# Performance work log

Measured on AMD Instinct MI355X. Metric: run time of the kernel, lower is better.

Reference implementation:

```python
import jax, jax.numpy as jnp
import numpy as np

D_MODEL = 256
NHEAD = 8
HEAD_DIM = D_MODEL // NHEAD
LN_EPS = 1e-5
NEG_INF = -1e30  # finite large-negative; avoids NaN rows while matching masked softmax


def setup_inputs() -> dict:
    key = jax.random.key(0)
    ks = jax.random.split(key, 9)
    B, Q, HW, D = 8, 100, 16384, D_MODEL
    s = 0.02
    return {
        "query": jax.random.normal(ks[0], (B, Q, D), jnp.float32),
        "key_value": jax.random.normal(ks[1], (B, HW, D), jnp.float32),
        "attn_mask": jax.random.randint(ks[2], (B * NHEAD, Q, HW), 0, 2) == 1,  # True = attend
        "in_proj_weight": jax.random.normal(ks[3], (3 * D, D), jnp.float32) * s,
        "in_proj_bias": jax.random.normal(ks[4], (3 * D,), jnp.float32) * s,
        "out_proj_weight": jax.random.normal(ks[5], (D, D), jnp.float32) * s,
        "out_proj_bias": jax.random.normal(ks[6], (D,), jnp.float32) * s,
        "ln_weight": jnp.ones((D,), jnp.float32),
        "ln_bias": jnp.zeros((D,), jnp.float32),
    }


def _mha_masked(query, key_value, attn_mask, in_proj_weight, in_proj_bias,
                out_proj_weight, out_proj_bias):
    B, Q, D = query.shape
    HW = key_value.shape[1]
    Wq, Wk, Wv = jnp.split(in_proj_weight, 3, axis=0)
    bq, bk, bv = jnp.split(in_proj_bias, 3, axis=0)
    q = (query @ Wq.T + bq).reshape(B, Q, NHEAD, HEAD_DIM)
    k = (key_value @ Wk.T + bk).reshape(B, HW, NHEAD, HEAD_DIM)
    v = (key_value @ Wv.T + bv).reshape(B, HW, NHEAD, HEAD_DIM)
    scale = 1.0 / np.sqrt(HEAD_DIM).astype(np.float32)
    scores = jnp.einsum("bqhd,bkhd->bhqk", q, k) * scale  # (B, H, Q, HW)
    attend = attn_mask.reshape(B, NHEAD, Q, HW)  # True = attend
    scores = jnp.where(attend, scores, NEG_INF)
    probs = jax.nn.softmax(scores, axis=-1)
    ctx = jnp.einsum("bhqk,bkhd->bqhd", probs, v).reshape(B, Q, D)
    return ctx @ out_proj_weight.T + out_proj_bias


def reference(query, key_value, attn_mask, in_proj_weight, in_proj_bias,
              out_proj_weight, out_proj_bias, ln_weight, ln_bias):
    attn_out = _mha_masked(query, key_value, attn_mask, in_proj_weight,
                           in_proj_bias, out_proj_weight, out_proj_bias)
    x = query + attn_out  # dropout p=0.0 is identity
    mu = jnp.mean(x, axis=-1, keepdims=True)
    var = jnp.mean(jnp.square(x - mu), axis=-1, keepdims=True)
    return (x - mu) * jax.lax.rsqrt(var + LN_EPS) * ln_weight + ln_bias
```

## Files before the change

### kernel.cpp

```cpp
#include <hip/hip_runtime.h>
#include <stdint.h>

#define BB   8
#define NH   8
#define QQ   100
#define HWK  16384
#define DM   256
#define HD   32
#define QP   112
#define MT   7
#define NPART 64
#define SCALE2 0.2550602534365564f

typedef short bf16x8 __attribute__((ext_vector_type(8)));
typedef float f32x4  __attribute__((ext_vector_type(4)));
typedef unsigned short u16;
typedef unsigned int   u32;
typedef unsigned long long u64;

__device__ __forceinline__ u16 f2bf(float f) {
  u32 u = __builtin_bit_cast(u32, f);
  u += 0x7fffu + ((u >> 16) & 1u);
  return (u16)(u >> 16);
}
__device__ __forceinline__ u16 f2bf_ru(float f) {
  return (u16)((__builtin_bit_cast(u32, f) + 0x8000u) >> 16);
}
__device__ __forceinline__ u32 pack2rn(float lo, float hi) {
  u32 a = __builtin_bit_cast(u32, lo) + 0x8000u;
  u32 b = __builtin_bit_cast(u32, hi) + 0x8000u;
  return __builtin_amdgcn_perm(b, a, 0x07060302u);
}
__device__ __forceinline__ float bf_lo(u32 u) {
  return __builtin_bit_cast(float, u << 16);
}
__device__ __forceinline__ float bf_hi(u32 u) {
  return __builtin_bit_cast(float, u & 0xffff0000u);
}
__device__ __forceinline__ float fast_exp2(float x) {
#if __has_builtin(__builtin_amdgcn_exp2f)
  return __builtin_amdgcn_exp2f(x);
#else
  return exp2f(x);
#endif
}

__global__ __launch_bounds__(256) void qw_kernel(
    const float* __restrict__ query, const float* __restrict__ W,
    const float* __restrict__ bias, u16* __restrict__ q_bf,
    u16* __restrict__ wbf) {
  __shared__ float xrow[DM];
  const int bid = blockIdx.x;
  const int tid = threadIdx.x;
  if (bid >= BB * QQ) {
    const int i = ((bid - BB * QQ) * 256 + tid) * 4;
    const float4 w = *(const float4*)(W + 256 * DM + i);
    u32* dst = (u32*)(wbf + i);
    dst[0] = pack2rn(w.x, w.y);
    dst[1] = pack2rn(w.z, w.w);
    return;
  }
  const int bq = bid;
  const int b = bq / QQ, qi = bq % QQ;
  if (tid < 64)
    ((float4*)xrow)[tid] = ((const float4*)(query + (size_t)bq * DM))[tid];
  __syncthreads();
  const int j = tid;
  float acc = bias[j];
  const float4* wr = (const float4*)(W + (size_t)j * DM);
  #pragma unroll 8
  for (int c = 0; c < 64; ++c) {
    float4 w = wr[c];
    float4 x = ((const float4*)xrow)[c];
    acc += w.x * x.x + w.y * x.y + w.z * x.z + w.w * x.w;
  }
  acc *= SCALE2;
  const int h = j >> 5, d = j & 31;
  q_bf[(((size_t)(b * NH + h)) * QQ + qi) * HD + d] = f2bf(acc);
}

__global__ __launch_bounds__(256) void kvcp_kernel(
    const float* __restrict__ kv, const u16* __restrict__ wbf,
    const float* __restrict__ bias, const int* __restrict__ mask,
    u16* __restrict__ k_bf, u16* __restrict__ v_t, u32* __restrict__ mbg) {
  __shared__ u16 Tl[4][5120];
  const int bid = blockIdx.x;
  const int tid = threadIdx.x, lane = tid & 63, wid = tid >> 6;

  if (bid % 3 == 2) {
    const int cpid = bid / 3;
    const int bh = cpid >> 4, chunk = cpid & 15;
    const int* mp_base = mask + (size_t)bh * QQ * HWK + chunk * 1024;
    u32* dst_base = mbg + (size_t)cpid * QP * 32;
    for (int rr = 0; rr < 25; ++rr) {
      const int row = wid * 25 + rr;
      const int* mp = mp_base + (size_t)row * HWK;
      int4 v[4];
      #pragma unroll
      for (int q = 0; q < 4; ++q) v[q] = ((const int4*)(mp + q * 256))[lane];
      #pragma unroll
      for (int q = 0; q < 4; ++q) {
        const u64 b0 = __ballot(v[q].x != 0);
        const u64 b1 = __ballot(v[q].y != 0);
        const u64 b2 = __ballot(v[q].z != 0);
        const u64 b3 = __ballot(v[q].w != 0);
        if (lane < 8) {
          const int j = lane >> 1;
          const u64 bj = (j == 0) ? b0 : (j == 1) ? b1 : (j == 2) ? b2 : b3;
          dst_base[row * 32 + q * 8 + (lane & 1) * 4 + j] =
              (lane & 1) ? (u32)(bj >> 32) : (u32)bj;
        }
      }
    }
    return;
  }

  const int rb = (bid / 3) * 2 + (bid % 3);
  const size_t m0 = (size_t)rb * 64;
  const int lane15 = lane & 15, quad = lane >> 4;
  const int jw = wid * 128;

  f32x4 acc[4][8];
  #pragma unroll
  for (int mi = 0; mi < 4; ++mi)
    #pragma unroll
    for (int ni = 0; ni < 8; ++ni) acc[mi][ni] = (f32x4){0.f, 0.f, 0.f, 0.f};

  for (int ks = 0; ks < 8; ++ks) {
    bf16x8 afr[4];
    #pragma unroll
    for (int mi = 0; mi < 4; ++mi) {
      const float* ap = kv + (m0 + mi * 16 + lane15) * DM + ks * 32 + quad * 8;
      float4 a0 = ((const float4*)ap)[0];
      float4 a1 = ((const float4*)ap)[1];
      uint4 w;
      w.x = pack2rn(a0.x, a0.y); w.y = pack2rn(a0.z, a0.w);
      w.z = pack2rn(a1.x, a1.y); w.w = pack2rn(a1.z, a1.w);
      afr[mi] = __builtin_bit_cast(bf16x8, w);
    }
    #pragma unroll
    for (int ni = 0; ni < 8; ++ni) {
      bf16x8 bfr = __builtin_bit_cast(bf16x8,
          *(const uint4*)(wbf + (size_t)(jw + ni * 16 + lane15) * DM + ks * 32 + quad * 8));
      #pragma unroll
      for (int mi = 0; mi < 4; ++mi)
        acc[mi][ni] = __builtin_amdgcn_mfma_f32_16x16x32_bf16(afr[mi], bfr, acc[mi][ni], 0, 0, 0);
    }
  }

  u16* T = Tl[wid];
  const float* bptr = bias + 256 + jw;
  if (wid < 2) {
    #pragma unroll
    for (int p = 0; p < 2; ++p) {
      #pragma unroll
      for (int mm = 0; mm < 2; ++mm) {
        const int mi = p * 2 + mm;
        #pragma unroll
        for (int ni = 0; ni < 8; ++ni) {
          const float bv = bptr[ni * 16 + lane15];
          #pragma unroll
          for (int r = 0; r < 4; ++r)
            T[(mm * 16 + quad * 4 + r) * 136 + ni * 16 + lane15] =
                f2bf_ru(acc[mi][ni][r] + bv);
        }
      }
      #pragma unroll
      for (int it = 0; it < 8; ++it) {
        const int row = it * 4 + quad;
        const int c0 = lane15 * 8;
        uint4 val = *(const uint4*)&T[row * 136 + c0];
        const size_t m = m0 + p * 32 + row;
        const size_t b = m >> 14, key = m & 16383;
        const int col256 = jw + c0;
        const int h = col256 >> 5, d = col256 & 31;
        *(uint4*)&k_bf[((b * NH + h) * HWK + key) * HD + d] = val;
      }
    }
  } else {
    const int jwv = jw - 256;
    #pragma unroll
    for (int p = 0; p < 2; ++p) {
      #pragma unroll
      for (int mm = 0; mm < 2; ++mm) {
        const int mi = p * 2 + mm;
        #pragma unroll
        for (int ni = 0; ni < 8; ++ni) {
          const float bv = bptr[ni * 16 + lane15];
          u32* dst = (u32*)&T[(ni * 16 + lane15) * 40 + mm * 16 + quad * 4];
          dst[0] = pack2rn(acc[mi][ni][0] + bv, acc[mi][ni][1] + bv);
          dst[1] = pack2rn(acc[mi][ni][2] + bv, acc[mi][ni][3] + bv);
        }
      }
      #pragma unroll
      for (int it = 0; it < 8; ++it) {
        const int col = it * 16 + (lane >> 2);
        const int koff = (lane & 3) * 8;
        uint4 val = *(const uint4*)&T[col * 40 + koff];
        const size_t m = m0 + p * 32 + koff;
        const size_t b = m >> 14, key = m & 16383;
        const int col256 = jwv + col;
        const int h = col256 >> 5, d = col256 & 31;
        *(uint4*)&v_t[((b * NH + h) * HD + d) * HWK + key] = val;
      }
    }
  }
}

__global__ __launch_bounds__(256) void attn_kernel(
    const u16* __restrict__ q_bf, const u16* __restrict__ k_bf,
    const u16* __restrict__ v_t, const u32* __restrict__ mbg,
    float* __restrict__ l_p, u32* __restrict__ ctxp) {
  const int tid = threadIdx.x;
  const int lane = tid & 63, wid = tid >> 6;
  const int lane15 = lane & 15, quad = lane >> 4;
  const int bh = blockIdx.x >> 4, chunk = blockIdx.x & 15;

  const int key_base = chunk * 1024 + wid * 256;
  const u16* kbase = k_bf + (size_t)bh * HWK * HD;
  const u16* vtb  = v_t  + (size_t)bh * HWK * HD;
  const u16* qb   = q_bf + (size_t)bh * QQ * HD;
  const u32* mrow = mbg + (size_t)blockIdx.x * QP * 32 + wid * 8;

  const int sl_lo = lane15 + 32 * (quad & 1);
  const int sl_hi = sl_lo + 16;
  const u32 selperm = (quad & 2) ? 0x07060302u : 0x05040100u;

  f32x4 acc[MT][2];
  float l_run[MT];
  #pragma unroll
  for (int mt = 0; mt < MT; ++mt) {
    acc[mt][0] = (f32x4){0.f, 0.f, 0.f, 0.f};
    acc[mt][1] = (f32x4){0.f, 0.f, 0.f, 0.f};
    l_run[mt] = 0.f;
  }

  for (int kg = 0; kg < 8; ++kg) {
    const int key0 = key_base + kg * 32;
    const int h4 = (kg & 4) ? 4 : 0;
    const int sh = ((kg & 3) << 3) + quad;
    bf16x8 kf0 = __builtin_bit_cast(bf16x8,
        *(const uint4*)(kbase + (size_t)(key0 + lane15) * HD + quad * 8));
    bf16x8 kf1 = __builtin_bit_cast(bf16x8,
        *(const uint4*)(kbase + (size_t)(key0 + 16 + lane15) * HD + quad * 8));
    bf16x8 vf0 = __builtin_bit_cast(bf16x8,
        *(const uint4*)(vtb + (size_t)lane15 * HWK + key0 + quad * 8));
    bf16x8 vf1 = __builtin_bit_cast(bf16x8,
        *(const uint4*)(vtb + (size_t)(lane15 + 16) * HWK + key0 + quad * 8));
    #pragma unroll
    for (int mt = 0; mt < MT; ++mt) {
      const int rowg = mt * 16 + lane15;
      bf16x8 af = __builtin_bit_cast(bf16x8,
          *(const uint4*)(qb + (size_t)rowg * HD + quad * 8));
      uint4 mwv = *(const uint4*)(mrow + rowg * 32 + h4);
      if (mt == MT - 1 && rowg >= QQ) mwv = (uint4){0u, 0u, 0u, 0u};
      const f32x4 zero = {0.f, 0.f, 0.f, 0.f};
      f32x4 s0 = __builtin_amdgcn_mfma_f32_16x16x32_bf16(kf0, af, zero, 0, 0, 0);
      f32x4 s1 = __builtin_amdgcn_mfma_f32_16x16x32_bf16(kf1, af, zero, 0, 0, 0);
      const u32 mw[4] = {mwv.x, mwv.y, mwv.z, mwv.w};
      u32 pk[4];
      float lsum = 0.f;
      #pragma unroll
      for (int r = 0; r < 4; ++r) {
        const float p0 = ((mw[r] >> sh) & 1u)       ? fast_exp2(s0[r]) : 0.f;
        const float p1 = ((mw[r] >> (sh + 4)) & 1u) ? fast_exp2(s1[r]) : 0.f;
        lsum += p0 + p1;
        pk[r] = pack2rn(p0, p1);
      }
      l_run[mt] += lsum;
      u32 wA0 = (u32)__shfl((int)pk[0], sl_lo);
      u32 wA1 = (u32)__shfl((int)pk[1], sl_lo);
      u32 wA2 = (u32)__shfl((int)pk[2], sl_lo);
      u32 wA3 = (u32)__shfl((int)pk[3], sl_lo);
      u32 wB0 = (u32)__shfl((int)pk[0], sl_hi);
      u32 wB1 = (u32)__shfl((int)pk[1], sl_hi);
      u32 wB2 = (u32)__shfl((int)pk[2], sl_hi);
      u32 wB3 = (u32)__shfl((int)pk[3], sl_hi);
      uint4 pw;
      pw.x = __builtin_amdgcn_perm(wA1, wA0, selperm);
      pw.y = __builtin_amdgcn_perm(wA3, wA2, selperm);
      pw.z = __builtin_amdgcn_perm(wB1, wB0, selperm);
      pw.w = __builtin_amdgcn_perm(wB3, wB2, selperm);
      bf16x8 pf = __builtin_bit_cast(bf16x8, pw);
      acc[mt][0] = __builtin_amdgcn_mfma_f32_16x16x32_bf16(vf0, pf, acc[mt][0], 0, 0, 0);
      acc[mt][1] = __builtin_amdgcn_mfma_f32_16x16x32_bf16(vf1, pf, acc[mt][1], 0, 0, 0);
    }
  }

  const int part = chunk * 4 + wid;
  #pragma unroll
  for (int mt = 0; mt < MT; ++mt) {
    const int row = mt * 16 + lane15;
    float lr = l_run[mt];
    lr += __shfl_xor(lr, 16);
    lr += __shfl_xor(lr, 32);
    const size_t base = ((size_t)bh * QP + row) * NPART + part;
    if (quad == 0) l_p[base] = lr;
    uint2 lo2, hi2;
    lo2.x = pack2rn(acc[mt][0][0], acc[mt][0][1]);
    lo2.y = pack2rn(acc[mt][0][2], acc[mt][0][3]);
    hi2.x = pack2rn(acc[mt][1][0], acc[mt][1][1]);
    hi2.y = pack2rn(acc[mt][1][2], acc[mt][1][3]);
    *(uint2*)&ctxp[base * 16 + quad * 2]     = lo2;
    *(uint2*)&ctxp[base * 16 + 8 + quad * 2] = hi2;
  }
}

__global__ __launch_bounds__(256) void combine_kernel(
    const float* __restrict__ l_p, const u32* __restrict__ ctxp,
    const float* __restrict__ query, const float* __restrict__ Wo,
    const float* __restrict__ bo, const float* __restrict__ lnw,
    const float* __restrict__ lnb, float* __restrict__ out) {
  __shared__ float ctx_row[DM];
  __shared__ float red[8];
  const int bq = blockIdx.x;
  const int b = bq / QQ, qi = bq % QQ;
  const int tid = threadIdx.x, lane = tid & 63, wid = tid >> 6;

  for (int hh = 0; hh < 2; ++hh) {
    const int h = wid * 2 + hh;
    const size_t base = ((size_t)(b * NH + h) * QP + qi) * NPART;
    float lv = l_p[base + lane];
    #pragma unroll
    for (int o = 1; o < 64; o <<= 1) lv += __shfl_xor(lv, o);
    const float inv_l = 1.0f / lv;
    const int c = lane & 7, pg = lane >> 3;
    const u32* cp = ctxp + base * 16 + c * 2;
    float s0 = 0.f, s1 = 0.f, s2 = 0.f, s3 = 0.f;
    for (int p = pg; p < NPART; p += 8) {
      uint2 u = *(const uint2*)(cp + (size_t)p * 16);
      s0 += bf_lo(u.x); s1 += bf_hi(u.x);
      s2 += bf_lo(u.y); s3 += bf_hi(u.y);
    }
    #pragma unroll
    for (int o = 8; o < 64; o <<= 1) {
      s0 += __shfl_xor(s0, o);
      s1 += __shfl_xor(s1, o);
      s2 += __shfl_xor(s2, o);
      s3 += __shfl_xor(s3, o);
    }
    if (pg == 0) {
      ctx_row[h * HD + c * 4]     = s0 * inv_l;
      ctx_row[h * HD + c * 4 + 1] = s1 * inv_l;
      ctx_row[h * HD + c * 4 + 2] = s2 * inv_l;
      ctx_row[h * HD + c * 4 + 3] = s3 * inv_l;
    }
  }
  __syncthreads();

  const int j = tid;
  float s = bo[j];
  const float4* wr = (const float4*)(Wo + (size_t)j * DM);
  #pragma unroll 8
  for (int c = 0; c < 64; ++c) {
    float4 wv = wr[c];
    float4 cx = ((const float4*)ctx_row)[c];
    s += wv.x * cx.x + wv.y * cx.y + wv.z * cx.z + wv.w * cx.w;
  }
  const float x = s + query[(size_t)bq * DM + j];

  float t = x;
  #pragma unroll
  for (int o = 1; o < 64; o <<= 1) t += __shfl_xor(t, o);
  if (lane == 0) red[wid] = t;
  __syncthreads();
  const float mu = (red[0] + red[1] + red[2] + red[3]) * (1.0f / DM);
  const float dx = x - mu;
  float t2 = dx * dx;
  #pragma unroll
  for (int o = 1; o < 64; o <<= 1) t2 += __shfl_xor(t2, o);
  if (lane == 0) red[4 + wid] = t2;
  __syncthreads();
  const float var = (red[4] + red[5] + red[6] + red[7]) * (1.0f / DM);
  out[(size_t)bq * DM + j] = dx * rsqrtf(var + 1e-5f) * lnw[j] + lnb[j];
}

extern "C" void kernel_launch(void* const* d_in, const int* in_sizes, int n_in,
                              void* d_out, int out_size, void* d_ws, size_t ws_size,
                              hipStream_t stream) {
  const float* query = (const float*)d_in[0];
  const float* kv    = (const float*)d_in[1];
  const int*   mask  = (const int*)d_in[2];
  const float* ipw   = (const float*)d_in[3];
  const float* ipb   = (const float*)d_in[4];
  const float* opw   = (const float*)d_in[5];
  const float* opb   = (const float*)d_in[6];
  const float* lnw   = (const float*)d_in[7];
  const float* lnb   = (const float*)d_in[8];
  float* out = (float*)d_out;

  char* ws = (char*)d_ws;
  u16*   k_bf  = (u16*)(ws);
  u16*   v_t   = (u16*)(ws + 67108864);
  u16*   q_bf  = (u16*)(ws + 134217728);
  float* l_p   = (float*)(ws + 134742016);
  u32*   ctxp  = (u32*)(ws + 136577024);
  u16*   wbf   = (u16*)(ws + 195297280);
  u32*   mbg   = (u32*)(ws + 195559424);

  qw_kernel     <<<BB * QQ + 128, 256, 0, stream>>>(query, ipw, ipb, q_bf, wbf);
  kvcp_kernel   <<<3072,          256, 0, stream>>>(kv, wbf, ipb, mask, k_bf, v_t, mbg);
  attn_kernel   <<<BB * NH * 16,  256, 0, stream>>>(q_bf, k_bf, v_t, mbg, l_p, ctxp);
  combine_kernel<<<BB * QQ,       256, 0, stream>>>(l_p, ctxp, query, opw, opb, lnw, lnb, out);
}
```

Before: 908.0 us.

## Move mask bit-packing into the Q kernel and stage KV tiles in LDS

The mask-to-bitmask packing moves from the KV projection kernel into the Q-projection kernel, so the K/V GEMM kernel handles only the projection. The KV kernel now uses 512-thread blocks that load a 64-row KV tile once, convert it to bf16 and store it in shared memory. All 8 waves then read from LDS, each covering 64 output columns, so KV is no longer read from global memory by every wave. The cost is more LDS per block and an extra barrier, and the Q kernel now carries the heavy mask-reading work.

```diff
diff --git a/kernel.cpp b/kernel.cpp
--- a/kernel.cpp
+++ b/kernel.cpp
@@ -47,48 +47,14 @@
 
 __global__ __launch_bounds__(256) void qw_kernel(
     const float* __restrict__ query, const float* __restrict__ W,
-    const float* __restrict__ bias, u16* __restrict__ q_bf,
-    u16* __restrict__ wbf) {
+    const float* __restrict__ bias, const int* __restrict__ mask,
+    u16* __restrict__ q_bf, u16* __restrict__ wbf, u32* __restrict__ mbg) {
   __shared__ float xrow[DM];
   const int bid = blockIdx.x;
-  const int tid = threadIdx.x;
-  if (bid >= BB * QQ) {
-    const int i = ((bid - BB * QQ) * 256 + tid) * 4;
-    const float4 w = *(const float4*)(W + 256 * DM + i);
-    u32* dst = (u32*)(wbf + i);
-    dst[0] = pack2rn(w.x, w.y);
-    dst[1] = pack2rn(w.z, w.w);
-    return;
-  }
-  const int bq = bid;
-  const int b = bq / QQ, qi = bq % QQ;
-  if (tid < 64)
-    ((float4*)xrow)[tid] = ((const float4*)(query + (size_t)bq * DM))[tid];
-  __syncthreads();
-  const int j = tid;
-  float acc = bias[j];
-  const float4* wr = (const float4*)(W + (size_t)j * DM);
-  #pragma unroll 8
-  for (int c = 0; c < 64; ++c) {
-    float4 w = wr[c];
-    float4 x = ((const float4*)xrow)[c];
-    acc += w.x * x.x + w.y * x.y + w.z * x.z + w.w * x.w;
-  }
-  acc *= SCALE2;
-  const int h = j >> 5, d = j & 31;
-  q_bf[(((size_t)(b * NH + h)) * QQ + qi) * HD + d] = f2bf(acc);
-}
-
-__global__ __launch_bounds__(256) void kvcp_kernel(
-    const float* __restrict__ kv, const u16* __restrict__ wbf,
-    const float* __restrict__ bias, const int* __restrict__ mask,
-    u16* __restrict__ k_bf, u16* __restrict__ v_t, u32* __restrict__ mbg) {
-  __shared__ u16 Tl[4][5120];
-  const int bid = blockIdx.x;
   const int tid = threadIdx.x, lane = tid & 63, wid = tid >> 6;
 
-  if (bid % 3 == 2) {
-    const int cpid = bid / 3;
+  if (bid < 1024) {
+    const int cpid = bid;
     const int bh = cpid >> 4, chunk = cpid & 15;
     const int* mp_base = mask + (size_t)bh * QQ * HWK + chunk * 1024;
     u32* dst_base = mbg + (size_t)cpid * QP * 32;
@@ -114,32 +80,69 @@
     }
     return;
   }
-
-  const int rb = (bid / 3) * 2 + (bid % 3);
+  if (bid >= 1024 + BB * QQ) {
+    const int i = ((bid - 1024 - BB * QQ) * 256 + tid) * 4;
+    const float4 w = *(const float4*)(W + 256 * DM + i);
+    u32* dst = (u32*)(wbf + i);
+    dst[0] = pack2rn(w.x, w.y);
+    dst[1] = pack2rn(w.z, w.w);
+    return;
+  }
+  const int bq = bid - 1024;
+  const int b = bq / QQ, qi = bq % QQ;
+  if (tid < 64)
+    ((float4*)xrow)[tid] = ((const float4*)(query + (size_t)bq * DM))[tid];
+  __syncthreads();
+  const int j = tid;
+  float acc = bias[j];
+  const float4* wr = (const float4*)(W + (size_t)j * DM);
+  #pragma unroll 8
+  for (int c = 0; c < 64; ++c) {
+    float4 w = wr[c];
+    float4 x = ((const float4*)xrow)[c];
+    acc += w.x * x.x + w.y * x.y + w.z * x.z + w.w * x.w;
+  }
+  acc *= SCALE2;
+  const int h = j >> 5, d = j & 31;
+  q_bf[(((size_t)(b * NH + h)) * QQ + qi) * HD + d] = f2bf(acc);
+}
+
+__global__ __launch_bounds__(512, 4) void kv_kernel(
+    const float* __restrict__ kv, const u16* __restrict__ wbf,
+    const float* __restrict__ bias, u16* __restrict__ k_bf,
+    u16* __restrict__ v_t) {
+  __shared__ u16 S[19456];
+  const int rb = blockIdx.x;
   const size_t m0 = (size_t)rb * 64;
+  const int tid = threadIdx.x, lane = tid & 63, wid = tid >> 6;
   const int lane15 = lane & 15, quad = lane >> 4;
-  const int jw = wid * 128;
-
-  f32x4 acc[4][8];
+  const int jw = wid * 64;
+
+  #pragma unroll
+  for (int t = 0; t < 8; ++t) {
+    const int idx = t * 512 + tid;
+    const int row = idx >> 6, c4 = idx & 63;
+    const float4 a = *(const float4*)(kv + (m0 + row) * DM + c4 * 4);
+    u32* dst = (u32*)&S[row * 264 + c4 * 4];
+    dst[0] = pack2rn(a.x, a.y);
+    dst[1] = pack2rn(a.z, a.w);
+  }
+  __syncthreads();
+
+  f32x4 acc[4][4];
   #pragma unroll
   for (int mi = 0; mi < 4; ++mi)
     #pragma unroll
-    for (int ni = 0; ni < 8; ++ni) acc[mi][ni] = (f32x4){0.f, 0.f, 0.f, 0.f};
+    for (int ni = 0; ni < 4; ++ni) acc[mi][ni] = (f32x4){0.f, 0.f, 0.f, 0.f};
 
   for (int ks = 0; ks < 8; ++ks) {
     bf16x8 afr[4];
     #pragma unroll
-    for (int mi = 0; mi < 4; ++mi) {
-      const float* ap = kv + (m0 + mi * 16 + lane15) * DM + ks * 32 + quad * 8;
-      float4 a0 = ((const float4*)ap)[0];
-      float4 a1 = ((const float4*)ap)[1];
-      uint4 w;
-      w.x = pack2rn(a0.x, a0.y); w.y = pack2rn(a0.z, a0.w);
-      w.z = pack2rn(a1.x, a1.y); w.w = pack2rn(a1.z, a1.w);
-      afr[mi] = __builtin_bit_cast(bf16x8, w);
-    }
-    #pragma unroll
-    for (int ni = 0; ni < 8; ++ni) {
+    for (int mi = 0; mi < 4; ++mi)
+      afr[mi] = __builtin_bit_cast(bf16x8,
+          *(const uint4*)&S[(mi * 16 + lane15) * 264 + ks * 32 + quad * 8]);
+    #pragma unroll
+    for (int ni = 0; ni < 4; ++ni) {
       bf16x8 bfr = __builtin_bit_cast(bf16x8,
           *(const uint4*)(wbf + (size_t)(jw + ni * 16 + lane15) * DM + ks * 32 + quad * 8));
       #pragma unroll
@@ -147,37 +150,39 @@
         acc[mi][ni] = __builtin_amdgcn_mfma_f32_16x16x32_bf16(afr[mi], bfr, acc[mi][ni], 0, 0, 0);
     }
   }
-
-  u16* T = Tl[wid];
+  __syncthreads();
+
   const float* bptr = bias + 256 + jw;
-  if (wid < 2) {
+  if (wid < 4) {
+    u16* T = S + wid * 2304;
     #pragma unroll
     for (int p = 0; p < 2; ++p) {
       #pragma unroll
       for (int mm = 0; mm < 2; ++mm) {
         const int mi = p * 2 + mm;
         #pragma unroll
-        for (int ni = 0; ni < 8; ++ni) {
+        for (int ni = 0; ni < 4; ++ni) {
           const float bv = bptr[ni * 16 + lane15];
           #pragma unroll
           for (int r = 0; r < 4; ++r)
-            T[(mm * 16 + quad * 4 + r) * 136 + ni * 16 + lane15] =
+            T[(mm * 16 + quad * 4 + r) * 72 + ni * 16 + lane15] =
                 f2bf_ru(acc[mi][ni][r] + bv);
         }
       }
       #pragma unroll
       for (int it = 0; it < 8; ++it) {
         const int row = it * 4 + quad;
-        const int c0 = lane15 * 8;
-        uint4 val = *(const uint4*)&T[row * 136 + c0];
+        const int c0 = lane15 * 4;
+        uint2 val = *(const uint2*)&T[row * 72 + c0];
         const size_t m = m0 + p * 32 + row;
         const size_t b = m >> 14, key = m & 16383;
         const int col256 = jw + c0;
         const int h = col256 >> 5, d = col256 & 31;
-        *(uint4*)&k_bf[((b * NH + h) * HWK + key) * HD + d] = val;
+        *(uint2*)&k_bf[((b * NH + h) * HWK + key) * HD + d] = val;
       }
     }
   } else {
+    u16* T = S + 9216 + (wid - 4) * 2560;
     const int jwv = jw - 256;
     #pragma unroll
     for (int p = 0; p < 2; ++p) {
@@ -185,7 +190,7 @@
       for (int mm = 0; mm < 2; ++mm) {
         const int mi = p * 2 + mm;
         #pragma unroll
-        for (int ni = 0; ni < 8; ++ni) {
+        for (int ni = 0; ni < 4; ++ni) {
           const float bv = bptr[ni * 16 + lane15];
           u32* dst = (u32*)&T[(ni * 16 + lane15) * 40 + mm * 16 + quad * 4];
           dst[0] = pack2rn(acc[mi][ni][0] + bv, acc[mi][ni][1] + bv);
@@ -193,7 +198,7 @@
         }
       }
       #pragma unroll
-      for (int it = 0; it < 8; ++it) {
+      for (int it = 0; it < 4; ++it) {
         const int col = it * 16 + (lane >> 2);
         const int koff = (lane & 3) * 8;
         uint4 val = *(const uint4*)&T[col * 40 + koff];
@@ -398,8 +403,8 @@
   u16*   wbf   = (u16*)(ws + 195297280);
   u32*   mbg   = (u32*)(ws + 195559424);
 
-  qw_kernel     <<<BB * QQ + 128, 256, 0, stream>>>(query, ipw, ipb, q_bf, wbf);
-  kvcp_kernel   <<<3072,          256, 0, stream>>>(kv, wbf, ipb, mask, k_bf, v_t, mbg);
-  attn_kernel   <<<BB * NH * 16,  256, 0, stream>>>(q_bf, k_bf, v_t, mbg, l_p, ctxp);
-  combine_kernel<<<BB * QQ,       256, 0, stream>>>(l_p, ctxp, query, opw, opb, lnw, lnb, out);
-}
+  qw_kernel     <<<1024 + BB * QQ + 128, 256, 0, stream>>>(query, ipw, ipb, mask, q_bf, wbf, mbg);
+  kv_kernel     <<<2048,                 512, 0, stream>>>(kv, wbf, ipb, k_bf, v_t);
+  attn_kernel   <<<BB * NH * 16,         256, 0, stream>>>(q_bf, k_bf, v_t, mbg, l_p, ctxp);
+  combine_kernel<<<BB * QQ,              256, 0, stream>>>(l_p, ctxp, query, opw, opb, lnw, lnb, out);
+}
```

New measurement: 822.9 us. 1.1x faster.
